# Kernel tuning notes

Measured on AMD Instinct MI355X. Metric: run time of the kernel, lower is better.

## Reference

```python
import jax, jax.numpy as jnp
import numpy as np


def setup_inputs() -> dict:
    key = jax.random.key(0)
    kx, kw = jax.random.split(key)
    x = jax.random.normal(kx, (32, 256, 56, 56), dtype=jnp.float32)
    # kaiming-uniform-like init for weights [O, I, K, K]
    fan_in = 256 * 3 * 3
    bound = float(np.sqrt(6.0 / fan_in))
    weights = jax.random.uniform(kw, (256, 256, 3, 3), dtype=jnp.float32,
                                 minval=-bound, maxval=bound)
    return {"x": x, "weights": weights}


def reference(x, weights):
    # Binarize weights with sign (STE is a backward-only concern; forward uses sign).
    qw = jnp.sign(weights)
    # conv2d, NCHW / OIHW, stride 1, no padding, no bias
    out = jax.lax.conv_general_dilated(
        x, qw,
        window_strides=(1, 1),
        padding="VALID",
        dimension_numbers=("NCHW", "OIHW", "NCHW"),
    )
    return out
```

## Files before the change

kernel.cpp:

```cpp
#include <hip/hip_runtime.h>
#include <cstdint>

#define NB 32
#define IC 256
#define OC 256
#define H 56
#define WIDTH 56
#define OH 54
#define OW 54
#define HW (H*WIDTH)
#define OHW (OH*OW)
#define KTOT 2304
#define M_TOT (NB*OHW)

#define BM 128
#define BO 128
#define BK 32
#define KSTEPS (KTOT/BK)
#define MBLOCKS (M_TOT/BM)

__device__ __align__(16) unsigned short g_qwt[2*KSTEPS*BO*BK];
__device__ __align__(16) unsigned short g_xq[NB*HW*IC];

typedef __bf16 bf16x8 __attribute__((ext_vector_type(8)));
typedef float  f32x4  __attribute__((ext_vector_type(4)));

typedef __attribute__((address_space(1))) const unsigned int gas_u32;
typedef __attribute__((address_space(3))) unsigned int las_u32;
__device__ __forceinline__ void async_copy16(const void* g, void* l) {
  __builtin_amdgcn_global_load_lds((gas_u32*)g, (las_u32*)l, 16, 0, 0);
}

__device__ inline unsigned short f32_bf16(float f) {
  union { float f; unsigned int u; } v; v.f = f;
  unsigned int u = v.u;
  return (unsigned short)((u + 0x7FFFu + ((u >> 16) & 1u)) >> 16);
}

__global__ __launch_bounds__(256) void repack_w(const float* __restrict__ w) {
  int L = blockIdx.x * 256 + threadIdx.x;
  int ob  = (L >= KSTEPS*BO*BK) ? 1 : 0;
  int rem = L - ob*(KSTEPS*BO*BK);
  int step = rem >> 12;
  int r    = (rem >> 5) & 127;
  int kc   = rem & 31;
  int o = ob*BO + r;
  int k = step*BK + kc;
  int pos = k >> 8;
  int c   = k & 255;
  int kh = pos / 3;
  int kw = pos - kh*3;
  float v = w[o*2304 + c*9 + kh*3 + kw];
  unsigned short s = (v > 0.f) ? 0x3F80u : ((v < 0.f) ? 0xBF80u : 0u);
  g_qwt[L] = s;
}

__global__ __launch_bounds__(256) void xform_x(const float* __restrict__ x) {
  __shared__ unsigned short tile[64][IC + 8];
  const int t   = threadIdx.x;
  const int n   = blockIdx.y;
  const int hw0 = blockIdx.x * 64;
  const int cl  = t >> 4;
  const int hl  = (t & 15) * 4;
  #pragma unroll 4
  for (int j = 0; j < 16; ++j) {
    int c = j*16 + cl;
    const float4 v = *(const float4*)(&x[(n*IC + c)*HW + hw0 + hl]);
    tile[hl+0][c] = f32_bf16(v.x);
    tile[hl+1][c] = f32_bf16(v.y);
    tile[hl+2][c] = f32_bf16(v.z);
    tile[hl+3][c] = f32_bf16(v.w);
  }
  __syncthreads();
  const int ch = (t & 31) * 8;
  const int hr = t >> 5;
  #pragma unroll
  for (int p = 0; p < 8; ++p) {
    int hwi = p*8 + hr;
    *(uint4*)(&g_xq[(n*HW + hw0 + hwi)*IC + ch]) = *(const uint4*)(&tile[hwi][ch]);
  }
}

__global__ __launch_bounds__(256) void bconv_gemm(float* __restrict__ out) {
  __shared__ __align__(16) unsigned short Wl[BO*BK];
  __shared__ __align__(16) unsigned short Xl[BM*BK];
  const int t  = threadIdx.x;
  const int m0 = blockIdx.x * BM;
  const int ob = blockIdx.y;

  int soff[2];
  #pragma unroll
  for (int hh = 0; hh < 2; ++hh) {
    int q = t + hh*256;
    int m = m0 + (q >> 2);
    int n  = m / OHW;
    int rm = m - n*OHW;
    int oh = rm / OW;
    int ow = rm - oh*OW;
    soff[hh] = ((n*H + oh)*WIDTH + ow)*IC + (q & 3)*8;
  }
  const unsigned short* wsrc = g_qwt + ob*(KSTEPS*BO*BK);

  const int lane = t & 63;
  const int wv   = t >> 6;
  const int col  = lane & 15;
  const int quad = lane >> 4;
  const int wo = (wv & 1) * 64;
  const int wm = (wv >> 1) * 64;
  int aoff[4], boff[4];
  #pragma unroll
  for (int i = 0; i < 4; ++i) {
    aoff[i] = (wo + i*16 + col)*BK + quad*8;
    boff[i] = (wm + i*16 + col)*BK + quad*8;
  }

  f32x4 acc[4][4];
  #pragma unroll
  for (int io = 0; io < 4; ++io)
    #pragma unroll
    for (int im = 0; im < 4; ++im)
      acc[io][im] = (f32x4){0.f, 0.f, 0.f, 0.f};

  for (int step = 0; step < KSTEPS; ++step) {
    const int k0  = step * BK;
    const int pos = k0 >> 8;
    const int c0  = k0 & 255;
    const int kh  = pos / 3;
    const int kw  = pos - kh*3;
    const int sk  = (kh*WIDTH + kw)*IC + c0;

    __syncthreads();
    async_copy16(&wsrc[step*(BO*BK) + t*8],         &Wl[t*8]);
    async_copy16(&wsrc[step*(BO*BK) + (t+256)*8],   &Wl[(t+256)*8]);
    async_copy16(&g_xq[soff[0] + sk],               &Xl[t*8]);
    async_copy16(&g_xq[soff[1] + sk],               &Xl[(t+256)*8]);
    __syncthreads();

    bf16x8 av[4], bv[4];
    #pragma unroll
    for (int i = 0; i < 4; ++i) av[i] = *(const bf16x8*)(&Wl[aoff[i]]);
    #pragma unroll
    for (int i = 0; i < 4; ++i) bv[i] = *(const bf16x8*)(&Xl[boff[i]]);

    #pragma unroll
    for (int io = 0; io < 4; ++io)
      #pragma unroll
      for (int im = 0; im < 4; ++im)
        acc[io][im] = __builtin_amdgcn_mfma_f32_16x16x32_bf16(av[io], bv[im], acc[io][im], 0, 0, 0);
  }

  #pragma unroll
  for (int im = 0; im < 4; ++im) {
    int m  = m0 + wm + im*16 + col;
    int n  = m / OHW;
    int rm = m - n*OHW;
    float* obase = out + n*(OC*OHW) + rm;
    #pragma unroll
    for (int io = 0; io < 4; ++io) {
      int orow = ob*BO + wo + io*16 + quad*4;
      #pragma unroll
      for (int r = 0; r < 4; ++r)
        obase[(orow + r)*OHW] = acc[io][im][r];
    }
  }
}

extern "C" void kernel_launch(void* const* d_in, const int* in_sizes, int n_in,
                              void* d_out, int out_size, void* d_ws, size_t ws_size,
                              hipStream_t stream) {
  const float* x = (const float*)d_in[0];
  const float* w = (const float*)d_in[1];
  float* out = (float*)d_out;

  repack_w<<<dim3((2*KSTEPS*BO*BK)/256), 256, 0, stream>>>(w);
  xform_x <<<dim3(HW/64, NB), 256, 0, stream>>>(x);
  bconv_gemm<<<dim3(MBLOCKS, 2), 256, 0, stream>>>(out);
}
```

Before: 358.6 us.

## Restructure binary conv as spatial-tile implicit GEMM with halo reuse in LDS

Replaces the im2col-style per-K-step gathering with a spatial tile: each block loads an 8x18 pixel halo patch of 32 channels into LDS once and reuses it across all 9 filter taps by shifting the LDS offset. Weights are now read directly from global memory (tap-major repacked layout) instead of being staged in LDS, and async global-to-LDS copies are replaced by plain vector loads and stores. This cuts redundant input loads by roughly the tap count. In exchange it adds overlapping tiles at the right edge (ow0=38 recomputes columns), a smaller 96-pixel output tile per block, and weight fragments fetched from global or L2 on every tap.

```diff
diff --git a/kernel.cpp b/kernel.cpp
--- a/kernel.cpp
+++ b/kernel.cpp
@@ -10,26 +10,17 @@
 #define OW 54
 #define HW (H*WIDTH)
 #define OHW (OH*OW)
-#define KTOT 2304
-#define M_TOT (NB*OHW)
 
-#define BM 128
-#define BO 128
-#define BK 32
-#define KSTEPS (KTOT/BK)
-#define MBLOCKS (M_TOT/BM)
+#define CBLK 8
+#define PXC 40
+#define PIH 8
+#define PIW 18
 
-__device__ __align__(16) unsigned short g_qwt[2*KSTEPS*BO*BK];
+__device__ __align__(16) unsigned short g_qwt[2*CBLK*9*128*32];
 __device__ __align__(16) unsigned short g_xq[NB*HW*IC];
 
 typedef __bf16 bf16x8 __attribute__((ext_vector_type(8)));
 typedef float  f32x4  __attribute__((ext_vector_type(4)));
-
-typedef __attribute__((address_space(1))) const unsigned int gas_u32;
-typedef __attribute__((address_space(3))) unsigned int las_u32;
-__device__ __forceinline__ void async_copy16(const void* g, void* l) {
-  __builtin_amdgcn_global_load_lds((gas_u32*)g, (las_u32*)l, 16, 0, 0);
-}
 
 __device__ inline unsigned short f32_bf16(float f) {
   union { float f; unsigned int u; } v; v.f = f;
@@ -39,18 +30,16 @@
 
 __global__ __launch_bounds__(256) void repack_w(const float* __restrict__ w) {
   int L = blockIdx.x * 256 + threadIdx.x;
-  int ob  = (L >= KSTEPS*BO*BK) ? 1 : 0;
-  int rem = L - ob*(KSTEPS*BO*BK);
-  int step = rem >> 12;
-  int r    = (rem >> 5) & 127;
-  int kc   = rem & 31;
-  int o = ob*BO + r;
-  int k = step*BK + kc;
-  int pos = k >> 8;
-  int c   = k & 255;
-  int kh = pos / 3;
-  int kw = pos - kh*3;
-  float v = w[o*2304 + c*9 + kh*3 + kw];
+  int img = L >> 12;
+  int o_  = (L >> 5) & 127;
+  int c_  = L & 31;
+  int tap = img % 9;
+  int t2  = img / 9;
+  int cb  = t2 & 7;
+  int ob  = t2 >> 3;
+  int o = ob*128 + o_;
+  int c = cb*32 + c_;
+  float v = w[o*2304 + c*9 + tap];
   unsigned short s = (v > 0.f) ? 0x3F80u : ((v < 0.f) ? 0xBF80u : 0u);
   g_qwt[L] = s;
 }
@@ -82,85 +71,101 @@
 }
 
 __global__ __launch_bounds__(256) void bconv_gemm(float* __restrict__ out) {
-  __shared__ __align__(16) unsigned short Wl[BO*BK];
-  __shared__ __align__(16) unsigned short Xl[BM*BK];
+  __shared__ __align__(16) unsigned short Xs[PIH*PIW*PXC];
   const int t  = threadIdx.x;
-  const int m0 = blockIdx.x * BM;
+  const int bx = blockIdx.x;
   const int ob = blockIdx.y;
 
-  int soff[2];
-  #pragma unroll
-  for (int hh = 0; hh < 2; ++hh) {
-    int q = t + hh*256;
-    int m = m0 + (q >> 2);
-    int n  = m / OHW;
-    int rm = m - n*OHW;
-    int oh = rm / OW;
-    int ow = rm - oh*OW;
-    soff[hh] = ((n*H + oh)*WIDTH + ow)*IC + (q & 3)*8;
+  const int ow_i = bx & 3;
+  const int t2   = bx >> 2;
+  const int oh_i = t2 % 9;
+  const int n    = t2 / 9;
+  const int oh0  = oh_i * 6;
+  const int ow0  = (ow_i == 3) ? 38 : ow_i * 16;
+
+  int src0, src1, src2 = 0, dst0, dst1, dst2 = 0;
+  {
+    int e, p, q, ih_l, iw_l;
+    e = t;        p = e >> 2; q = e & 3; ih_l = p / PIW; iw_l = p - ih_l*PIW;
+    src0 = ((n*H + oh0 + ih_l)*WIDTH + ow0 + iw_l)*IC + q*8;
+    dst0 = p*PXC + q*8;
+    e = t + 256;  p = e >> 2; q = e & 3; ih_l = p / PIW; iw_l = p - ih_l*PIW;
+    src1 = ((n*H + oh0 + ih_l)*WIDTH + ow0 + iw_l)*IC + q*8;
+    dst1 = p*PXC + q*8;
+    if (t < 64) {
+      e = t + 512; p = e >> 2; q = e & 3; ih_l = p / PIW; iw_l = p - ih_l*PIW;
+      src2 = ((n*H + oh0 + ih_l)*WIDTH + ow0 + iw_l)*IC + q*8;
+      dst2 = p*PXC + q*8;
+    }
   }
-  const unsigned short* wsrc = g_qwt + ob*(KSTEPS*BO*BK);
 
   const int lane = t & 63;
   const int wv   = t >> 6;
   const int col  = lane & 15;
   const int quad = lane >> 4;
-  const int wo = (wv & 1) * 64;
-  const int wm = (wv >> 1) * 64;
-  int aoff[4], boff[4];
+  const int wo   = (wv & 1) * 64;
+  const int mh   = wv >> 1;
+
+  int aoff[4];
   #pragma unroll
-  for (int i = 0; i < 4; ++i) {
-    aoff[i] = (wo + i*16 + col)*BK + quad*8;
-    boff[i] = (wm + i*16 + col)*BK + quad*8;
-  }
+  for (int i = 0; i < 4; ++i) aoff[i] = (wo + i*16 + col)*32 + quad*8;
+  int boff[3];
+  #pragma unroll
+  for (int i = 0; i < 3; ++i) boff[i] = ((3*mh + i)*PIW + col)*PXC + quad*8;
 
-  f32x4 acc[4][4];
+  const unsigned short* wbase = g_qwt + ob*(CBLK*9*4096);
+
+  f32x4 acc[4][3];
   #pragma unroll
   for (int io = 0; io < 4; ++io)
     #pragma unroll
-    for (int im = 0; im < 4; ++im)
+    for (int im = 0; im < 3; ++im)
       acc[io][im] = (f32x4){0.f, 0.f, 0.f, 0.f};
 
-  for (int step = 0; step < KSTEPS; ++step) {
-    const int k0  = step * BK;
-    const int pos = k0 >> 8;
-    const int c0  = k0 & 255;
-    const int kh  = pos / 3;
-    const int kw  = pos - kh*3;
-    const int sk  = (kh*WIDTH + kw)*IC + c0;
-
+  for (int cb = 0; cb < CBLK; ++cb) {
+    const int csh = cb * 32;
     __syncthreads();
-    async_copy16(&wsrc[step*(BO*BK) + t*8],         &Wl[t*8]);
-    async_copy16(&wsrc[step*(BO*BK) + (t+256)*8],   &Wl[(t+256)*8]);
-    async_copy16(&g_xq[soff[0] + sk],               &Xl[t*8]);
-    async_copy16(&g_xq[soff[1] + sk],               &Xl[(t+256)*8]);
+    {
+      uint4 v0 = *(const uint4*)(&g_xq[src0 + csh]);
+      uint4 v1 = *(const uint4*)(&g_xq[src1 + csh]);
+      uint4 v2;
+      if (t < 64) v2 = *(const uint4*)(&g_xq[src2 + csh]);
+      *(uint4*)(&Xs[dst0]) = v0;
+      *(uint4*)(&Xs[dst1]) = v1;
+      if (t < 64) *(uint4*)(&Xs[dst2]) = v2;
+    }
     __syncthreads();
 
-    bf16x8 av[4], bv[4];
+    const unsigned short* wimg = wbase + cb*(9*4096);
     #pragma unroll
-    for (int i = 0; i < 4; ++i) av[i] = *(const bf16x8*)(&Wl[aoff[i]]);
-    #pragma unroll
-    for (int i = 0; i < 4; ++i) bv[i] = *(const bf16x8*)(&Xl[boff[i]]);
-
-    #pragma unroll
-    for (int io = 0; io < 4; ++io)
+    for (int tap = 0; tap < 9; ++tap) {
+      const int kh = tap / 3, kw = tap % 3;
+      bf16x8 av[4], bv[3];
       #pragma unroll
-      for (int im = 0; im < 4; ++im)
-        acc[io][im] = __builtin_amdgcn_mfma_f32_16x16x32_bf16(av[io], bv[im], acc[io][im], 0, 0, 0);
+      for (int i = 0; i < 4; ++i)
+        av[i] = *(const bf16x8*)(wimg + tap*4096 + aoff[i]);
+      #pragma unroll
+      for (int i = 0; i < 3; ++i)
+        bv[i] = *(const bf16x8*)(&Xs[boff[i] + (kh*PIW + kw)*PXC]);
+      #pragma unroll
+      for (int io = 0; io < 4; ++io)
+        #pragma unroll
+        for (int im = 0; im < 3; ++im)
+          acc[io][im] = __builtin_amdgcn_mfma_f32_16x16x32_bf16(av[io], bv[im], acc[io][im], 0, 0, 0);
+    }
   }
 
   #pragma unroll
-  for (int im = 0; im < 4; ++im) {
-    int m  = m0 + wm + im*16 + col;
-    int n  = m / OHW;
-    int rm = m - n*OHW;
-    float* obase = out + n*(OC*OHW) + rm;
+  for (int im = 0; im < 3; ++im) {
+    const int oh = oh0 + 3*mh + im;
+    const int ow = ow0 + col;
     #pragma unroll
     for (int io = 0; io < 4; ++io) {
-      int orow = ob*BO + wo + io*16 + quad*4;
+      const int o = ob*128 + wo + io*16 + quad*4;
+      float* p = out + ((n*OC + o)*OH + oh)*OW + ow;
       #pragma unroll
       for (int r = 0; r < 4; ++r)
-        obase[(orow + r)*OHW] = acc[io][im][r];
+        p[r*OHW] = acc[io][im][r];
     }
   }
 }
@@ -172,7 +177,7 @@
   const float* w = (const float*)d_in[1];
   float* out = (float*)d_out;
 
-  repack_w<<<dim3((2*KSTEPS*BO*BK)/256), 256, 0, stream>>>(w);
+  repack_w<<<dim3(589824/256), 256, 0, stream>>>(w);
   xform_x <<<dim3(HW/64, NB), 256, 0, stream>>>(x);
-  bconv_gemm<<<dim3(MBLOCKS, 2), 256, 0, stream>>>(out);
+  bconv_gemm<<<dim3(NB*9*4, 2), 256, 0, stream>>>(out);
 }
```

New measurement: 414.9 us. +15.7%, slower.
